# Kernel tuning notes

Hardware: AMD Instinct MI355X
Metric: run time of the kernel (lower is better)

## Reference

```python
import jax, jax.numpy as jnp
import numpy as np

E = 576        # embed_dims
HEADS = 18
NPTS = 12
NF = 3         # num_frames
DD = 2 * NF - 1  # depth of value volume (5)
HD = E // HEADS  # head dim (32)


def _grid_init_bias():
    # Faithful reproduction of init_weights() for sampling_offsets.bias
    theta = np.arange(8) * (2.0 * np.pi / 8)
    yaw = np.stack([np.cos(theta), np.sin(theta), np.zeros(8)], -1)
    roll = np.stack([np.zeros(8), np.cos(theta), np.sin(theta)], -1)
    pitch = np.stack([np.cos(theta), np.zeros(8), np.sin(theta)], -1)
    g = np.concatenate([yaw, pitch[[1, 2, 3, 5, 6, 7]], roll[[1, 3, 5, 7]]], 0)  # (18,3)
    g = g / np.abs(g).max(-1, keepdims=True)
    g = np.tile(g[:, None, None, :], (1, 1, NPTS, 1))              # (18,1,12,3)
    g = g * np.arange(1, NPTS + 1, dtype=np.float64)[None, None, :, None]
    return g.reshape(-1).astype(np.float32)                        # (18*12*3,)


def setup_inputs() -> dict:
    key = jax.random.key(0)
    ks = jax.random.split(key, 6)
    bs, h, w = 2, 64, 80
    nq = h * w
    lim = float(np.sqrt(6.0 / (E + E)))  # xavier uniform for square E x E
    return {
        "query": jax.random.normal(ks[0], (bs, nq, E), jnp.float32),
        "value": jax.random.normal(ks[1], (bs, nq * DD, E), jnp.float32),
        "query_pos": jax.random.normal(ks[2], (bs, nq, E), jnp.float32),
        "W_off": jnp.zeros((E, HEADS * NPTS * 3), jnp.float32),  # constant_init 0
        "b_off": jnp.asarray(_grid_init_bias()),
        "W_attn": jnp.zeros((E, HEADS * NPTS), jnp.float32),
        "b_attn": jnp.zeros((HEADS * NPTS,), jnp.float32),
        "W_v": jax.random.uniform(ks[3], (E, E), jnp.float32, -lim, lim),
        "b_v": jnp.zeros((E,), jnp.float32),
        "W_out": jax.random.uniform(ks[4], (E, E), jnp.float32, -lim, lim),
        "b_out": jnp.zeros((E,), jnp.float32),
        "h": 64,
        "w": 80,
    }


def _deform_attn_3d(value, loc, attn, D, H, W):
    # value: (bs, D*H*W, heads, hd)  token order: depth-major (D, H, W)
    # loc:   (bs, nq, heads, np, 3)  normalized (x, y, z) in [0,1]
    # attn:  (bs, nq, heads, np)
    bs, _, heads, hd = value.shape
    nq = loc.shape[1]
    # (bs, heads, D*H*W, hd) flat spatial for gathers
    v = value.reshape(bs, D, H, W, heads, hd).transpose(0, 4, 1, 2, 3, 5)
    v = v.reshape(bs, heads, D * H * W, hd)
    lt = jnp.moveaxis(loc, 2, 1)    # (bs, heads, nq, np, 3)
    at = jnp.moveaxis(attn, 2, 1)   # (bs, heads, nq, np)
    # grid_sample(align_corners=False) coordinate convention: pix = u*size - 0.5
    x = lt[..., 0] * W - 0.5
    y = lt[..., 1] * H - 0.5
    z = lt[..., 2] * D - 0.5
    x0 = jnp.floor(x); y0 = jnp.floor(y); z0 = jnp.floor(z)
    fx = x - x0; fy = y - y0; fz = z - z0
    acc = jnp.zeros((bs, heads, nq, NPTS, hd), v.dtype)
    for dz in (0, 1):
        for dy in (0, 1):
            for dx in (0, 1):
                xi = x0 + dx; yi = y0 + dy; zi = z0 + dz
                wgt = ((fx if dx else 1.0 - fx)
                       * (fy if dy else 1.0 - fy)
                       * (fz if dz else 1.0 - fz))
                valid = ((xi >= 0) & (xi < W) & (yi >= 0) & (yi < H)
                         & (zi >= 0) & (zi < D))
                xc = jnp.clip(xi, 0, W - 1).astype(jnp.int32)
                yc = jnp.clip(yi, 0, H - 1).astype(jnp.int32)
                zc = jnp.clip(zi, 0, D - 1).astype(jnp.int32)
                idx = ((zc * H + yc) * W + xc).reshape(bs, heads, nq * NPTS)
                g = jnp.take_along_axis(v, idx[..., None], axis=2)
                g = g.reshape(bs, heads, nq, NPTS, hd)
                acc = acc + g * (wgt * valid.astype(v.dtype))[..., None]
    out = jnp.einsum("bhqp,bhqpd->bhqd", at, acc)  # softmax-weighted sum over points
    return out.transpose(0, 2, 1, 3).reshape(bs, nq, heads * hd)


def _forward(query, value, query_pos, W_off, b_off, W_attn, b_attn,
             W_v, b_v, W_out, b_out, h, w):
    bs, nq, _ = query.shape
    q = query + query_pos
    v = (value @ W_v + b_v).reshape(bs, nq * DD, HEADS, HD)
    offs = (q @ W_off + b_off).reshape(bs, nq, HEADS, NPTS, 3)
    attn = jax.nn.softmax((q @ W_attn + b_attn).reshape(bs, nq, HEADS, NPTS), axis=-1)
    # reference points: pixel centers normalized, z = 0
    ry, rx = jnp.meshgrid((jnp.arange(h, dtype=jnp.float32) + 0.5) / h,
                          (jnp.arange(w, dtype=jnp.float32) + 0.5) / w,
                          indexing="ij")
    ref = jnp.stack([rx.reshape(-1), ry.reshape(-1),
                     jnp.zeros(h * w, jnp.float32)], -1)  # (nq, 3)
    norm = jnp.array([w, h, NF], jnp.float32)  # NOTE: z normalized by num_frames (as in source)
    loc = ref[None, :, None, None, :] + offs / norm
    out = _deform_attn_3d(v, loc, attn, DD, h, w)
    return out @ W_out + b_out  # dropout is identity at eval


def reference(query, value, query_pos, W_off, b_off, W_attn, b_attn,
              W_v, b_v, W_out, b_out, h, w):
    return _forward(query, value, query_pos, W_off, b_off, W_attn, b_attn,
                    W_v, b_v, W_out, b_out, h, w)
```

## Files before the change

kernel.cpp:

```cpp
#include <hip/hip_runtime.h>
#include <cstdint>

#define E_DIM   576
#define HEADS   18
#define NPTS    12
#define DDEPTH  5
#define HDIM    32
#define BSZ     2
#define GH      64
#define GW      80
#define NQ      (GH*GW)
#define NTOK    (NQ*DDEPTH)
#define MIXW    864
#define BQ_TOT  (BSZ*NQ)

typedef __attribute__((ext_vector_type(8))) short short8;
typedef __attribute__((ext_vector_type(4))) float f32x4;

__device__ __forceinline__ float b2f_lo(uint32_t u) {
    union { uint32_t u; float f; } v; v.u = u << 16; return v.f;
}
__device__ __forceinline__ float b2f_hi(uint32_t u) {
    union { uint32_t u; float f; } v; v.u = u & 0xffff0000u; return v.f;
}
__device__ __forceinline__ ushort f2b(float f) {
    union { float f; uint32_t u; } v; v.f = f;
    return (ushort)((v.u + 0x7fffu + ((v.u >> 16) & 1u)) >> 16);
}

__global__ void cast_kernel(const float* __restrict__ in, ushort* __restrict__ out, int n4) {
    int i = blockIdx.x * blockDim.x + threadIdx.x;
    if (i >= n4) return;
    const float4 v = reinterpret_cast<const float4*>(in)[i];
    ushort4 o; o.x = f2b(v.x); o.y = f2b(v.y); o.z = f2b(v.z); o.w = f2b(v.w);
    reinterpret_cast<ushort4*>(out)[i] = o;
}

__global__ void cast_add_kernel(const float* __restrict__ a, const float* __restrict__ b,
                                ushort* __restrict__ out, int n4) {
    int i = blockIdx.x * blockDim.x + threadIdx.x;
    if (i >= n4) return;
    const float4 va = reinterpret_cast<const float4*>(a)[i];
    const float4 vb = reinterpret_cast<const float4*>(b)[i];
    ushort4 o;
    o.x = f2b(va.x + vb.x); o.y = f2b(va.y + vb.y);
    o.z = f2b(va.z + vb.z); o.w = f2b(va.w + vb.w);
    reinterpret_cast<ushort4*>(out)[i] = o;
}

__global__ void prep_weights(const float* __restrict__ W_v, const float* __restrict__ W_out,
                             const float* __restrict__ W_off, const float* __restrict__ W_attn,
                             const float* __restrict__ b_off, const float* __restrict__ b_attn,
                             ushort* __restrict__ wt_v, ushort* __restrict__ wt_out,
                             ushort* __restrict__ wt_mix, float* __restrict__ bias_mix) {
    int idx = blockIdx.x * blockDim.x + threadIdx.x;
    if (idx < 864) bias_mix[idx] = (idx < 648) ? b_off[idx] : b_attn[idx - 648];
    if (idx < 331776) {
        int n = idx / E_DIM, k = idx - n * E_DIM;
        wt_v[idx] = f2b(W_v[(size_t)k * E_DIM + n]);
    } else if (idx < 663552) {
        int j = idx - 331776;
        int n = j / E_DIM, k = j - n * E_DIM;
        wt_out[j] = f2b(W_out[(size_t)k * E_DIM + n]);
    } else if (idx < 1161216) {
        int j = idx - 663552;
        int n = j / E_DIM, k = j - n * E_DIM;
        float v = (n < 648) ? W_off[(size_t)k * 648 + n] : W_attn[(size_t)k * 216 + (n - 648)];
        wt_mix[j] = f2b(v);
    }
}

#define TM 128
#define TN 96
#define BK 32

__device__ __forceinline__ void async_cp16(const ushort* gsrc, ushort* ldst) {
    __builtin_amdgcn_global_load_lds(
        (const __attribute__((address_space(1))) void*)gsrc,
        (__attribute__((address_space(3))) void*)ldst, 16, 0, 0);
}

template <typename OutT>
__global__ void gemm_mfma(const ushort* __restrict__ A, const ushort* __restrict__ Bt,
                          const float* __restrict__ bias, OutT* __restrict__ C,
                          int M, int N, int K, int ldc) {
    __shared__ __align__(16) ushort Asb[2][TM * BK];
    __shared__ __align__(16) ushort Bsb[2][TN * BK];
    const int tid  = threadIdx.x;
    const int wave = tid >> 6;
    const int lane = tid & 63;
    const int m16  = lane & 15;
    const int quad = lane >> 4;
    const int wr   = wave >> 1;
    const int wc   = wave & 1;
    const int row0 = blockIdx.x * TM;
    const int n0   = blockIdx.y * TN;

    const f32x4 zero = {0.f, 0.f, 0.f, 0.f};
    f32x4 acc[4][3];
    #pragma unroll
    for (int rt = 0; rt < 4; ++rt)
        #pragma unroll
        for (int ct = 0; ct < 3; ++ct) acc[rt][ct] = zero;

    const int srow = lane >> 2;
    const int scol = (((lane & 3) ^ ((lane >> 3) & 3))) * 8;
    const int ksw  = (quad ^ ((m16 >> 1) & 3)) * 8;

    auto stage = [&](int buf, int k0) {
        #pragma unroll
        for (int c = 0; c < 2; ++c) {
            const int ch = wave + c * 4;
            async_cp16(A + (size_t)(row0 + ch * 16 + srow) * K + k0 + scol,
                       &Asb[buf][ch * 512 + lane * 8]);
        }
        async_cp16(Bt + (size_t)(n0 + wave * 16 + srow) * K + k0 + scol,
                   &Bsb[buf][wave * 512 + lane * 8]);
        if (wave < 2)
            async_cp16(Bt + (size_t)(n0 + (wave + 4) * 16 + srow) * K + k0 + scol,
                       &Bsb[buf][(wave + 4) * 512 + lane * 8]);
    };

    stage(0, 0);
    __syncthreads();

    int cur = 0;
    for (int k0 = 0; k0 < K; k0 += BK) {
        if (k0 + BK < K) stage(cur ^ 1, k0 + BK);

        short8 afrag[4], bfrag[3];
        #pragma unroll
        for (int rt = 0; rt < 4; ++rt)
            afrag[rt] = *reinterpret_cast<const short8*>(
                &Asb[cur][(wr * 4 + rt) * 512 + m16 * 32 + ksw]);
        #pragma unroll
        for (int ct = 0; ct < 3; ++ct)
            bfrag[ct] = *reinterpret_cast<const short8*>(
                &Bsb[cur][(wc * 3 + ct) * 512 + m16 * 32 + ksw]);

        #pragma unroll
        for (int rt = 0; rt < 4; ++rt)
            #pragma unroll
            for (int ct = 0; ct < 3; ++ct)
                acc[rt][ct] = __builtin_amdgcn_mfma_f32_16x16x32_bf16(
                    afrag[rt], bfrag[ct], acc[rt][ct], 0, 0, 0);

        __syncthreads();
        cur ^= 1;
    }

    #pragma unroll
    for (int ct = 0; ct < 3; ++ct) {
        const int col = n0 + wc * 48 + ct * 16 + m16;
        const float bcol = bias[col];
        #pragma unroll
        for (int rt = 0; rt < 4; ++rt) {
            #pragma unroll
            for (int r = 0; r < 4; ++r) {
                const int row = row0 + wr * 64 + rt * 16 + quad * 4 + r;
                const float val = acc[rt][ct][r] + bcol;
                if constexpr (__is_same(OutT, float)) {
                    C[(size_t)row * ldc + col] = val;
                } else {
                    C[(size_t)row * ldc + col] = f2b(val);
                }
            }
        }
    }
}

__global__ void __launch_bounds__(256, 8)
deform_kernel(const ushort* __restrict__ vbuf,
              const float* __restrict__ mix,
              ushort* __restrict__ aout) {
    const int gl   = threadIdx.x >> 4;
    const int l    = threadIdx.x & 15;
    const int head = blockIdx.x / 640;
    const int bq   = (blockIdx.x % 640) * 16 + gl;
    const int q    = bq % NQ;
    const int b    = bq / NQ;
    const int qx   = q % GW;
    const int qy   = q / GW;

    const float* mrow = mix + (size_t)bq * MIXW;

    float lg = (l < NPTS) ? mrow[648 + head * NPTS + l] : -1e30f;
    float mx = lg;
    #pragma unroll
    for (int mk = 1; mk < 16; mk <<= 1) mx = fmaxf(mx, __shfl_xor(mx, mk, 16));
    float e = (l < NPTS) ? __expf(lg - mx) : 0.f;
    float s = e;
    #pragma unroll
    for (int mk = 1; mk < 16; mk <<= 1) s += __shfl_xor(s, mk, 16);

    float    cw[8];
    uint32_t coff[8];
    uint32_t mask = 0;
    {
        const float ap = e / s;
        const int pl = (l < NPTS) ? l : 0;
        const int ob = (head * NPTS + pl) * 3;
        const float ox = mrow[ob + 0];
        const float oy = mrow[ob + 1];
        const float oz = mrow[ob + 2];
        const float x = (float)qx + ox;
        const float y = (float)qy + oy;
        const float z = oz * (5.0f / 3.0f) - 0.5f;
        const float x0f = floorf(x), y0f = floorf(y), z0f = floorf(z);
        const int x0 = (int)x0f, y0 = (int)y0f, z0 = (int)z0f;
        const float fx = x - x0f, fy = y - y0f, fz = z - z0f;

        #pragma unroll
        for (int dz = 0; dz < 2; ++dz) {
            const int zi = z0 + dz;
            const bool zv = (zi >= 0) & (zi < DDEPTH);
            const int zc = min(max(zi, 0), DDEPTH - 1);
            const float wz = dz ? fz : 1.f - fz;
            #pragma unroll
            for (int dy = 0; dy < 2; ++dy) {
                const int yi = y0 + dy;
                const bool yv = (yi >= 0) & (yi < GH);
                const int yc = min(max(yi, 0), GH - 1);
                const float wy = dy ? fy : 1.f - fy;
                #pragma unroll
                for (int dx = 0; dx < 2; ++dx) {
                    const int xi = x0 + dx;
                    const bool xv = (xi >= 0) & (xi < GW);
                    const int xc = min(max(xi, 0), GW - 1);
                    const float wx = dx ? fx : 1.f - fx;
                    const int i = dz * 4 + dy * 2 + dx;
                    const bool valid = zv & yv & xv & (l < NPTS);
                    cw[i]   = ap * wz * wy * wx;
                    coff[i] = (uint32_t)((zc * GH + yc) * GW + xc) * (E_DIM / 2);
                    mask |= (valid ? (1u << i) : 0u);
                }
            }
        }
    }

    const uint32_t* vb = reinterpret_cast<const uint32_t*>(vbuf)
                         + (size_t)b * NTOK * (E_DIM / 2) + head * (HDIM / 2) + l;
    float o0 = 0.f, o1 = 0.f;
    #pragma unroll
    for (int p = 0; p < NPTS; ++p) {
        const uint32_t msk = (uint32_t)__shfl((int)mask, p, 16);
        if (msk == 0) continue;
        #pragma unroll
        for (int i = 0; i < 8; ++i) {
            if (msk & (1u << i)) {
                const float    w   = __shfl(cw[i], p, 16);
                const uint32_t off = (uint32_t)__shfl((int)coff[i], p, 16);
                const uint32_t pair = vb[off];
                o0 += w * b2f_lo(pair);
                o1 += w * b2f_hi(pair);
            }
        }
    }
    const uint32_t packed = (uint32_t)f2b(o0) | ((uint32_t)f2b(o1) << 16);
    reinterpret_cast<uint32_t*>(aout)[(size_t)bq * (E_DIM / 2) + head * (HDIM / 2) + l] = packed;
}

extern "C" void kernel_launch(void* const* d_in, const int* in_sizes, int n_in,
                              void* d_out, int out_size, void* d_ws, size_t ws_size,
                              hipStream_t stream) {
    const float* query     = (const float*)d_in[0];
    const float* value     = (const float*)d_in[1];
    const float* query_pos = (const float*)d_in[2];
    const float* W_off     = (const float*)d_in[3];
    const float* b_off     = (const float*)d_in[4];
    const float* W_attn    = (const float*)d_in[5];
    const float* b_attn    = (const float*)d_in[6];
    const float* W_v       = (const float*)d_in[7];
    const float* b_v       = (const float*)d_in[8];
    const float* W_out     = (const float*)d_in[9];
    const float* b_out     = (const float*)d_in[10];
    float* out = (float*)d_out;

    char* ws = (char*)d_ws;
    ushort* vbuf     = (ushort*)(ws);
    ushort* val_bf16 = (ushort*)(ws + 58982400);
    ushort* aout     = val_bf16;
    ushort* q_bf16   = (ushort*)(ws + 117964800);
    float*  mixb     = (float*) (ws + 129761280);
    ushort* wt_v     = (ushort*)(ws + 165150720);
    ushort* wt_out   = (ushort*)(ws + 165814272);
    ushort* wt_mix   = (ushort*)(ws + 166477824);
    float*  bias_mix = (float*) (ws + 167473152);

    cast_kernel<<<(51200 * 576 / 4 + 255) / 256, 256, 0, stream>>>(value, val_bf16, 51200 * 576 / 4);
    cast_add_kernel<<<(10240 * 576 / 4 + 255) / 256, 256, 0, stream>>>(query, query_pos, q_bf16, 10240 * 576 / 4);
    prep_weights<<<(1161216 + 255) / 256, 256, 0, stream>>>(
        W_v, W_out, W_off, W_attn, b_off, b_attn, wt_v, wt_out, wt_mix, bias_mix);

    gemm_mfma<float><<<dim3(10240 / TM, MIXW / TN), 256, 0, stream>>>(
        q_bf16, wt_mix, bias_mix, mixb, BSZ * NQ, MIXW, E_DIM, MIXW);

    gemm_mfma<ushort><<<dim3(51200 / TM, E_DIM / TN), 256, 0, stream>>>(
        val_bf16, wt_v, b_v, vbuf, BSZ * NTOK, E_DIM, E_DIM, E_DIM);

    deform_kernel<<<HEADS * 640, 256, 0, stream>>>(vbuf, mixb, aout);

    gemm_mfma<float><<<dim3(10240 / TM, E_DIM / TN), 256, 0, stream>>>(
        aout, wt_out, b_out, out, BSZ * NQ, E_DIM, E_DIM, E_DIM);
}
```

Baseline: 398.0 us.

## Fuse fp32-to-bf16 casts and query+pos add into GEMM A-tile loads

```diff
diff --git a/kernel.cpp b/kernel.cpp
--- a/kernel.cpp
+++ b/kernel.cpp
@@ -16,6 +16,7 @@
 
 typedef __attribute__((ext_vector_type(8))) short short8;
 typedef __attribute__((ext_vector_type(4))) float f32x4;
+typedef __attribute__((ext_vector_type(4))) uint32_t u32x4;
 
 __device__ __forceinline__ float b2f_lo(uint32_t u) {
     union { uint32_t u; float f; } v; v.u = u << 16; return v.f;
@@ -27,25 +28,8 @@
     union { float f; uint32_t u; } v; v.f = f;
     return (ushort)((v.u + 0x7fffu + ((v.u >> 16) & 1u)) >> 16);
 }
-
-__global__ void cast_kernel(const float* __restrict__ in, ushort* __restrict__ out, int n4) {
-    int i = blockIdx.x * blockDim.x + threadIdx.x;
-    if (i >= n4) return;
-    const float4 v = reinterpret_cast<const float4*>(in)[i];
-    ushort4 o; o.x = f2b(v.x); o.y = f2b(v.y); o.z = f2b(v.z); o.w = f2b(v.w);
-    reinterpret_cast<ushort4*>(out)[i] = o;
-}
-
-__global__ void cast_add_kernel(const float* __restrict__ a, const float* __restrict__ b,
-                                ushort* __restrict__ out, int n4) {
-    int i = blockIdx.x * blockDim.x + threadIdx.x;
-    if (i >= n4) return;
-    const float4 va = reinterpret_cast<const float4*>(a)[i];
-    const float4 vb = reinterpret_cast<const float4*>(b)[i];
-    ushort4 o;
-    o.x = f2b(va.x + vb.x); o.y = f2b(va.y + vb.y);
-    o.z = f2b(va.z + vb.z); o.w = f2b(va.w + vb.w);
-    reinterpret_cast<ushort4*>(out)[i] = o;
+__device__ __forceinline__ uint32_t pkbf(float a, float b) {
+    return (uint32_t)f2b(a) | ((uint32_t)f2b(b) << 16);
 }
 
 __global__ void prep_weights(const float* __restrict__ W_v, const float* __restrict__ W_out,
@@ -74,14 +58,19 @@
 #define TN 96
 #define BK 32
 
+#define AM_BF16   0
+#define AM_F32    1
+#define AM_F32ADD 2
+
 __device__ __forceinline__ void async_cp16(const ushort* gsrc, ushort* ldst) {
     __builtin_amdgcn_global_load_lds(
         (const __attribute__((address_space(1))) void*)gsrc,
         (__attribute__((address_space(3))) void*)ldst, 16, 0, 0);
 }
 
-template <typename OutT>
-__global__ void gemm_mfma(const ushort* __restrict__ A, const ushort* __restrict__ Bt,
+template <int AMODE, typename OutT>
+__global__ void gemm_mfma(const void* __restrict__ Apv, const float* __restrict__ A2,
+                          const ushort* __restrict__ Bt,
                           const float* __restrict__ bias, OutT* __restrict__ C,
                           int M, int N, int K, int ldc) {
     __shared__ __align__(16) ushort Asb[2][TM * BK];
@@ -93,8 +82,8 @@
     const int quad = lane >> 4;
     const int wr   = wave >> 1;
     const int wc   = wave & 1;
-    const int row0 = blockIdx.x * TM;
-    const int n0   = blockIdx.y * TN;
+    const int row0 = blockIdx.y * TM;
+    const int n0   = blockIdx.x * TN;
 
     const f32x4 zero = {0.f, 0.f, 0.f, 0.f};
     f32x4 acc[4][3];
@@ -107,13 +96,55 @@
     const int scol = (((lane & 3) ^ ((lane >> 3) & 3))) * 8;
     const int ksw  = (quad ^ ((m16 >> 1) & 3)) * 8;
 
-    auto stage = [&](int buf, int k0) {
+    const int srow_f = ((wave & 1) << 6) | lane;
+    const int khalf  = wave >> 1;
+    const float* A32  = (const float*)Apv;
+    const ushort* A16 = (const ushort*)Apv;
+    const float* arow  = A32 + (size_t)(row0 + srow_f) * K + khalf * 16;
+    const float* arow2 = (AMODE == AM_F32ADD)
+                         ? A2 + (size_t)(row0 + srow_f) * K + khalf * 16 : nullptr;
+
+    float4 av0, av1, av2, av3;
+    float4 bv0, bv1, bv2, bv3;
+
+    auto issueA = [&](int k0) {
+        av0 = *reinterpret_cast<const float4*>(arow + k0);
+        av1 = *reinterpret_cast<const float4*>(arow + k0 + 4);
+        av2 = *reinterpret_cast<const float4*>(arow + k0 + 8);
+        av3 = *reinterpret_cast<const float4*>(arow + k0 + 12);
+        if constexpr (AMODE == AM_F32ADD) {
+            bv0 = *reinterpret_cast<const float4*>(arow2 + k0);
+            bv1 = *reinterpret_cast<const float4*>(arow2 + k0 + 4);
+            bv2 = *reinterpret_cast<const float4*>(arow2 + k0 + 8);
+            bv3 = *reinterpret_cast<const float4*>(arow2 + k0 + 12);
+        }
+    };
+    auto writeA = [&](int buf) {
+        float4 v0 = av0, v1 = av1, v2 = av2, v3 = av3;
+        if constexpr (AMODE == AM_F32ADD) {
+            v0.x += bv0.x; v0.y += bv0.y; v0.z += bv0.z; v0.w += bv0.w;
+            v1.x += bv1.x; v1.y += bv1.y; v1.z += bv1.z; v1.w += bv1.w;
+            v2.x += bv2.x; v2.y += bv2.y; v2.z += bv2.z; v2.w += bv2.w;
+            v3.x += bv3.x; v3.y += bv3.y; v3.z += bv3.z; v3.w += bv3.w;
+        }
+        const int r  = srow_f & 15;
+        const int ck = srow_f >> 4;
+        const int xr = (r >> 1) & 3;
+        const int s0 = khalf * 2;
+        u32x4 w0 = {pkbf(v0.x, v0.y), pkbf(v0.z, v0.w), pkbf(v1.x, v1.y), pkbf(v1.z, v1.w)};
+        u32x4 w1 = {pkbf(v2.x, v2.y), pkbf(v2.z, v2.w), pkbf(v3.x, v3.y), pkbf(v3.z, v3.w)};
+        *reinterpret_cast<u32x4*>(&Asb[buf][ck * 512 + r * 32 + ((s0 ^ xr) * 8)]) = w0;
+        *reinterpret_cast<u32x4*>(&Asb[buf][ck * 512 + r * 32 + (((s0 + 1) ^ xr) * 8)]) = w1;
+    };
+    auto stageA_lds = [&](int buf, int k0) {
         #pragma unroll
         for (int c = 0; c < 2; ++c) {
             const int ch = wave + c * 4;
-            async_cp16(A + (size_t)(row0 + ch * 16 + srow) * K + k0 + scol,
+            async_cp16(A16 + (size_t)(row0 + ch * 16 + srow) * K + k0 + scol,
                        &Asb[buf][ch * 512 + lane * 8]);
         }
+    };
+    auto stageB = [&](int buf, int k0) {
         async_cp16(Bt + (size_t)(n0 + wave * 16 + srow) * K + k0 + scol,
                    &Bsb[buf][wave * 512 + lane * 8]);
         if (wave < 2)
@@ -121,12 +152,24 @@
                        &Bsb[buf][(wave + 4) * 512 + lane * 8]);
     };
 
-    stage(0, 0);
+    if constexpr (AMODE == AM_BF16) {
+        stageA_lds(0, 0);
+        stageB(0, 0);
+    } else {
+        issueA(0);
+        stageB(0, 0);
+        writeA(0);
+    }
     __syncthreads();
 
     int cur = 0;
     for (int k0 = 0; k0 < K; k0 += BK) {
-        if (k0 + BK < K) stage(cur ^ 1, k0 + BK);
+        const bool nx = (k0 + BK < K);
+        if constexpr (AMODE == AM_BF16) {
+            if (nx) { stageA_lds(cur ^ 1, k0 + BK); stageB(cur ^ 1, k0 + BK); }
+        } else {
+            if (nx) { issueA(k0 + BK); stageB(cur ^ 1, k0 + BK); }
+        }
 
         short8 afrag[4], bfrag[3];
         #pragma unroll
@@ -145,6 +188,9 @@
                 acc[rt][ct] = __builtin_amdgcn_mfma_f32_16x16x32_bf16(
                     afrag[rt], bfrag[ct], acc[rt][ct], 0, 0, 0);
 
+        if constexpr (AMODE != AM_BF16) {
+            if (nx) writeA(cur ^ 1);
+        }
         __syncthreads();
         cur ^= 1;
     }
@@ -278,28 +324,24 @@
 
     char* ws = (char*)d_ws;
     ushort* vbuf     = (ushort*)(ws);
-    ushort* val_bf16 = (ushort*)(ws + 58982400);
-    ushort* aout     = val_bf16;
-    ushort* q_bf16   = (ushort*)(ws + 117964800);
-    float*  mixb     = (float*) (ws + 129761280);
-    ushort* wt_v     = (ushort*)(ws + 165150720);
-    ushort* wt_out   = (ushort*)(ws + 165814272);
-    ushort* wt_mix   = (ushort*)(ws + 166477824);
-    float*  bias_mix = (float*) (ws + 167473152);
-
-    cast_kernel<<<(51200 * 576 / 4 + 255) / 256, 256, 0, stream>>>(value, val_bf16, 51200 * 576 / 4);
-    cast_add_kernel<<<(10240 * 576 / 4 + 255) / 256, 256, 0, stream>>>(query, query_pos, q_bf16, 10240 * 576 / 4);
+    ushort* aout     = (ushort*)(ws + 58982400);
+    float*  mixb     = (float*) (ws + 70778880);
+    ushort* wt_v     = (ushort*)(ws + 106168320);
+    ushort* wt_out   = (ushort*)(ws + 106831872);
+    ushort* wt_mix   = (ushort*)(ws + 107495424);
+    float*  bias_mix = (float*) (ws + 108490752);
+
     prep_weights<<<(1161216 + 255) / 256, 256, 0, stream>>>(
         W_v, W_out, W_off, W_attn, b_off, b_attn, wt_v, wt_out, wt_mix, bias_mix);
 
-    gemm_mfma<float><<<dim3(10240 / TM, MIXW / TN), 256, 0, stream>>>(
-        q_bf16, wt_mix, bias_mix, mixb, BSZ * NQ, MIXW, E_DIM, MIXW);
-
-    gemm_mfma<ushort><<<dim3(51200 / TM, E_DIM / TN), 256, 0, stream>>>(
-        val_bf16, wt_v, b_v, vbuf, BSZ * NTOK, E_DIM, E_DIM, E_DIM);
+    gemm_mfma<AM_F32ADD, float><<<dim3(MIXW / TN, BQ_TOT / TM), 256, 0, stream>>>(
+        query, query_pos, wt_mix, bias_mix, mixb, BQ_TOT, MIXW, E_DIM, MIXW);
+
+    gemm_mfma<AM_F32, ushort><<<dim3(E_DIM / TN, (BSZ * NTOK) / TM), 256, 0, stream>>>(
+        value, nullptr, wt_v, b_v, vbuf, BSZ * NTOK, E_DIM, E_DIM, E_DIM);
 
     deform_kernel<<<HEADS * 640, 256, 0, stream>>>(vbuf, mixb, aout);
 
-    gemm_mfma<float><<<dim3(10240 / TM, E_DIM / TN), 256, 0, stream>>>(
-        aout, wt_out, b_out, out, BSZ * NQ, E_DIM, E_DIM, E_DIM);
-}
+    gemm_mfma<AM_BF16, float><<<dim3(E_DIM / TN, BQ_TOT / TM), 256, 0, stream>>>(
+        aout, nullptr, wt_out, b_out, out, BQ_TOT, E_DIM, E_DIM, E_DIM);
+}
```

New measurement: 507.2 us. 1.27x slower.
